# Kernel tuning notes

Measured on AMD Instinct MI355X. Metric: run time of the kernel, lower is better.

The kernel has to match this reference:

```python
import jax, jax.numpy as jnp
import numpy as np

N_TRACK, N_INTER, D, E = 100000, 50000, 64, 800000


def setup_inputs() -> dict:
    key = jax.random.key(0)
    ks = jax.random.split(key, 24)
    f32 = jnp.float32
    def w(k, i, o):
        return jax.random.normal(k, (i, o), f32) / np.float32(np.sqrt(i))
    def b(k, o):
        return jax.random.normal(k, (o,), f32) * np.float32(0.01)
    return {
        "x_track": jax.random.normal(ks[0], (N_TRACK, D), f32),
        "x_inter": jax.random.normal(ks[1], (N_INTER, D), f32),
        "W_conv_ti": w(ks[2], D, D), "b_conv_ti": b(ks[3], D),
        "W_conv_it": w(ks[4], D, D), "b_conv_it": b(ks[5], D),
        "W_att_track": w(ks[6], 3 * D, 3 * D), "b_att_track": b(ks[7], 3 * D),
        "W_aggr_track": w(ks[8], 3 * D, D), "b_aggr_track": b(ks[9], D),
        "W_att_inter": w(ks[10], 3 * D, 3 * D), "b_att_inter": b(ks[11], 3 * D),
        "W_aggr_inter": w(ks[12], 3 * D, D), "b_aggr_inter": b(ks[13], D),
        "W_self_track": w(ks[14], 2 * D, D), "b_self_track": b(ks[15], D),
        "W_self_inter": w(ks[16], 2 * D, D), "b_self_inter": b(ks[17], D),
        "src_ti": jax.random.randint(ks[18], (E,), 0, N_TRACK),
        "dst_ti": jax.random.randint(ks[19], (E,), 0, N_INTER),
        "src_it": jax.random.randint(ks[20], (E,), 0, N_INTER),
        "dst_it": jax.random.randint(ks[21], (E,), 0, N_TRACK),
    }


def _multi_aggregate(msgs, dst_idx, n_dst):
    # torch: scatter_add (sum), sum/count.clamp(1) (mean), scatter_reduce amax
    # over a zeros baseline with include_self=True -> max(0, segment_max).
    s = jax.ops.segment_sum(msgs, dst_idx, num_segments=n_dst)
    cnt = jax.ops.segment_sum(jnp.ones((msgs.shape[0], 1), msgs.dtype), dst_idx,
                              num_segments=n_dst)
    mean = s / jnp.maximum(cnt, 1.0)
    mx = jnp.maximum(jax.ops.segment_max(msgs, dst_idx, num_segments=n_dst), 0.0)
    return jnp.concatenate([mean, s, mx], axis=1)  # aggr order: mean, sum, max


def _dst_update(total, W_att, b_att, W_aggr, b_aggr):
    mask = jnp.sum(jnp.abs(total), axis=1) == 0  # nodes with no messages
    att = jax.nn.sigmoid(total @ W_att + b_att)
    out = (total * att) @ W_aggr + b_aggr
    return jnp.where(mask[:, None], 0.0, out)


def _selfloop(out, x, W_s, b_s):
    out = jax.nn.leaky_relu(out)  # wrapper leaky_relu on conv output
    mask = jnp.sum(jnp.abs(out), axis=1) == 0
    y = jax.nn.leaky_relu(jnp.concatenate([out, x], axis=1) @ W_s + b_s)
    return jnp.where(mask[:, None], x, y)  # masked fallback: keep input rows


def _forward(x_track, x_inter,
             W_conv_ti, b_conv_ti, W_conv_it, b_conv_it,
             W_att_track, b_att_track, W_aggr_track, b_aggr_track,
             W_att_inter, b_att_inter, W_aggr_inter, b_aggr_inter,
             W_self_track, b_self_track, W_self_inter, b_self_inter,
             src_ti, dst_ti, src_it, dst_it):
    # NoAggGAT message: lin(x_j) gathered along edges [E, D]
    msg_ti = x_track[src_ti] @ W_conv_ti + b_conv_ti   # track -> intermediate
    msg_it = x_inter[src_it] @ W_conv_it + b_conv_it   # intermediate -> track
    tot_inter = _multi_aggregate(msg_ti, dst_ti, x_inter.shape[0])  # [N_i, 3D]
    tot_track = _multi_aggregate(msg_it, dst_it, x_track.shape[0])  # [N_t, 3D]
    out_inter = _dst_update(tot_inter, W_att_inter, b_att_inter,
                            W_aggr_inter, b_aggr_inter)
    out_track = _dst_update(tot_track, W_att_track, b_att_track,
                            W_aggr_track, b_aggr_track)
    out_track = _selfloop(out_track, x_track, W_self_track, b_self_track)
    out_inter = _selfloop(out_inter, x_inter, W_self_inter, b_self_inter)
    return jnp.concatenate([out_track, out_inter], axis=0)  # [N_t + N_i, D]


def reference(x_track, x_inter,
              W_conv_ti, b_conv_ti, W_conv_it, b_conv_it,
              W_att_track, b_att_track, W_aggr_track, b_aggr_track,
              W_att_inter, b_att_inter, W_aggr_inter, b_aggr_inter,
              W_self_track, b_self_track, W_self_inter, b_self_inter,
              src_ti, dst_ti, src_it, dst_it):
    return _forward(x_track, x_inter,
                    W_conv_ti, b_conv_ti, W_conv_it, b_conv_it,
                    W_att_track, b_att_track, W_aggr_track, b_aggr_track,
                    W_att_inter, b_att_inter, W_aggr_inter, b_aggr_inter,
                    W_self_track, b_self_track, W_self_inter, b_self_inter,
                    src_ti, dst_ti, src_it, dst_it)
```

## Files before the change

### kernel.cpp

```cpp
#include <hip/hip_runtime.h>
#include <hip/hip_bf16.h>
#include <cstdio>
#include <cstdint>

#define DD 64
#define EPT 8

typedef __attribute__((ext_vector_type(8))) short bf16x8;
typedef __attribute__((ext_vector_type(4))) float f32x4;

__device__ __forceinline__ short f2b(float f) {
    __hip_bfloat16 h = __float2bfloat16(f);
    return __builtin_bit_cast(short, h);
}
__device__ __forceinline__ float b2f(unsigned short s) {
    unsigned u = ((unsigned)s) << 16;
    return __builtin_bit_cast(float, u);
}

__global__ void transform_mfma(const float* __restrict__ xt, const short* __restrict__ WTt,
                               const float* __restrict__ bt, unsigned short* __restrict__ yt, int ntk,
                               const float* __restrict__ xi, const short* __restrict__ WTi,
                               const float* __restrict__ bi, unsigned short* __restrict__ yi, int nik) {
    const float* x; const short* WT; const float* b; unsigned short* y; int n;
    if (blockIdx.y == 0) { x = xt; WT = WTt; b = bt; y = yt; n = ntk; }
    else                 { x = xi; WT = WTi; b = bi; y = yi; n = nik; }
    const int tid = threadIdx.x;
    const int wave = tid >> 6, lane = tid & 63;
    const int lr = lane & 15, lg = lane >> 4;
    const int row0 = blockIdx.x * 256 + wave * 64;
    if (row0 >= n) return;

    bf16x8 B[4][2];
    #pragma unroll
    for (int nt = 0; nt < 4; ++nt)
        #pragma unroll
        for (int ks = 0; ks < 2; ++ks)
            B[nt][ks] = *(const bf16x8*)&WT[(size_t)(nt * 16 + lr) * 64 + ks * 32 + lg * 8];
    float bias[4];
    #pragma unroll
    for (int nt = 0; nt < 4; ++nt) bias[nt] = b[nt * 16 + lr];

    f32x4 acc[4][4];
    f32x4 z4 = {0.f, 0.f, 0.f, 0.f};
    #pragma unroll
    for (int rt = 0; rt < 4; ++rt)
        #pragma unroll
        for (int nt = 0; nt < 4; ++nt) acc[rt][nt] = z4;

    #pragma unroll
    for (int rt = 0; rt < 4; ++rt) {
        int r = row0 + rt * 16 + lr;
        #pragma unroll
        for (int ks = 0; ks < 2; ++ks) {
            bf16x8 af = {0, 0, 0, 0, 0, 0, 0, 0};
            if (r < n) {
                const float* p = &x[(size_t)r * 64 + ks * 32 + lg * 8];
                float4 u0 = *(const float4*)p;
                float4 u1 = *(const float4*)(p + 4);
                af[0] = f2b(u0.x); af[1] = f2b(u0.y); af[2] = f2b(u0.z); af[3] = f2b(u0.w);
                af[4] = f2b(u1.x); af[5] = f2b(u1.y); af[6] = f2b(u1.z); af[7] = f2b(u1.w);
            }
            #pragma unroll
            for (int nt = 0; nt < 4; ++nt)
                acc[rt][nt] = __builtin_amdgcn_mfma_f32_16x16x32_bf16(af, B[nt][ks], acc[rt][nt], 0, 0, 0);
        }
    }
    #pragma unroll
    for (int rt = 0; rt < 4; ++rt)
        #pragma unroll
        for (int j = 0; j < 4; ++j) {
            int r = row0 + rt * 16 + lg * 4 + j;
            if (r >= n) continue;
            #pragma unroll
            for (int nt = 0; nt < 4; ++nt)
                y[(size_t)r * 64 + nt * 16 + lr] = (unsigned short)f2b(acc[rt][nt][j] + bias[nt]);
        }
}

__global__ void hist_part(const int* __restrict__ dti, const int* __restrict__ dit, int E,
                          int* __restrict__ rin, int* __restrict__ rtr, int nin, int ntr) {
    const int* dst = blockIdx.y ? dit : dti;
    int* row       = blockIdx.y ? rtr : rin;
    int n          = blockIdx.y ? ntr : nin;
    int part  = blockIdx.x & 7;
    int chunk = blockIdx.x >> 3;
    int psz = (n + 7) >> 3;
    int lo = part * psz, hi = min(n, lo + psz);
    int base = chunk * (256 * EPT) + threadIdx.x;
    #pragma unroll
    for (int k = 0; k < EPT; ++k) {
        int i = base + k * 256;
        if (i < E) {
            int d = dst[i];
            if (d >= lo && d < hi) atomicAdd(&row[d + 1], 1);
        }
    }
}

#define SCHUNK 4096
__global__ void scan_p1(int* __restrict__ rowA, int nA, int* __restrict__ bsA,
                        int* __restrict__ rowB, int nB, int* __restrict__ bsB) {
    int* row = blockIdx.y ? rowB : rowA;
    int n    = blockIdx.y ? nB : nA;
    int* bs  = blockIdx.y ? bsB : bsA;
    int b = blockIdx.x, t = threadIdx.x;
    int base = 1 + b * SCHUNK;
    __shared__ int wsum[4];
    if (base > n) { if (t == 0) bs[b] = 0; return; }
    int idx0 = base + t * 16;
    int v[16];
    int s = 0;
    #pragma unroll
    for (int k = 0; k < 16; ++k) {
        int i = idx0 + k;
        int x = (i <= n) ? row[i] : 0;
        s += x; v[k] = s;
    }
    int lane = t & 63, wid = t >> 6;
    int ssc = s;
    #pragma unroll
    for (int off = 1; off < 64; off <<= 1) {
        int u = __shfl_up(ssc, off, 64);
        if (lane >= off) ssc += u;
    }
    if (lane == 63) wsum[wid] = ssc;
    __syncthreads();
    int wprev = 0;
    #pragma unroll
    for (int w = 0; w < 4; ++w) if (w < wid) wprev += wsum[w];
    int tpre = ssc - s + wprev;
    #pragma unroll
    for (int k = 0; k < 16; ++k) {
        int i = idx0 + k;
        if (i <= n) row[i] = v[k] + tpre;
    }
    if (t == 0) bs[b] = wsum[0] + wsum[1] + wsum[2] + wsum[3];
}

__global__ void scan_p2(int* __restrict__ bsA, int* __restrict__ bsB) {
    int* bs = blockIdx.x ? bsB : bsA;
    int lane = threadIdx.x;
    int v = bs[lane];
    int s = v;
    #pragma unroll
    for (int off = 1; off < 64; off <<= 1) {
        int u = __shfl_up(s, off, 64);
        if (lane >= off) s += u;
    }
    bs[lane] = s - v;
}

__global__ void scan_p3(int* __restrict__ rowA, int* __restrict__ curA, int nA,
                        const int* __restrict__ bsA,
                        int* __restrict__ rowB, int* __restrict__ curB, int nB,
                        const int* __restrict__ bsB) {
    int* row = blockIdx.y ? rowB : rowA;
    int* cur = blockIdx.y ? curB : curA;
    int n    = blockIdx.y ? nB : nA;
    const int* bs = blockIdx.y ? bsB : bsA;
    int b = blockIdx.x, t = threadIdx.x;
    int base = 1 + b * SCHUNK;
    if (b == 0 && t == 0) { row[0] = 0; cur[0] = 0; }
    if (base > n) return;
    int off = bs[b];
    int end = min(base + SCHUNK - 1, n);
    for (int i = base + t; i <= end; i += 256) {
        int val = row[i] + off;
        row[i] = val;
        if (i < n) cur[i] = val;
    }
}

__global__ void permute_part(const int* __restrict__ sti, const int* __restrict__ dti,
                             int* __restrict__ cin, int* __restrict__ oti,
                             const int* __restrict__ sit, const int* __restrict__ dit,
                             int* __restrict__ ctr, int* __restrict__ oit,
                             int E, int nin, int ntr) {
    const int* src; const int* dst; int* cur; int* col; int n;
    if (blockIdx.y == 0) { src = sti; dst = dti; cur = cin; col = oti; n = nin; }
    else                 { src = sit; dst = dit; cur = ctr; col = oit; n = ntr; }
    int part  = blockIdx.x & 7;
    int chunk = blockIdx.x >> 3;
    int psz = (n + 7) >> 3;
    int lo = part * psz, hi = min(n, lo + psz);
    int base = chunk * (256 * EPT) + threadIdx.x;
    #pragma unroll
    for (int k = 0; k < EPT; ++k) {
        int i = base + k * 256;
        if (i < E) {
            int d = dst[i];
            if (d >= lo && d < hi) {
                int p = atomicAdd(&cur[d], 1);
                col[p] = src[i];
            }
        }
    }
}

__global__ void aggregate2(const unsigned short* __restrict__ yt, const int* __restrict__ row_in,
                           const int* __restrict__ col_ti, short* __restrict__ tot_in,
                           int* __restrict__ flag_in, int n_in,
                           const unsigned short* __restrict__ yi, const int* __restrict__ row_tr,
                           const int* __restrict__ col_it, short* __restrict__ tot_tr,
                           int* __restrict__ flag_tr, int n_tr) {
    const unsigned short* y; const int* row; const int* col; short* tot; int* flag; int n;
    if (blockIdx.y == 0) { y = yt; row = row_in; col = col_ti; tot = tot_in; flag = flag_in; n = n_in; }
    else                 { y = yi; row = row_tr; col = col_it; tot = tot_tr; flag = flag_tr; n = n_tr; }
    int wv = (int)((blockIdx.x * (size_t)blockDim.x + threadIdx.x) >> 6);
    if (wv >= n) return;
    int lane = threadIdx.x & 63;
    int sub = lane >> 4;
    int dl4 = (lane & 15) * 4;
    int e0 = row[wv], e1 = row[wv + 1];
    float s0 = 0.f, s1 = 0.f, s2 = 0.f, s3 = 0.f;
    float m0 = 0.f, m1 = 0.f, m2 = 0.f, m3 = 0.f;
    int e = e0 + sub;
    for (; e + 12 < e1; e += 16) {
        int c0 = col[e], c1 = col[e + 4], c2 = col[e + 8], c3 = col[e + 12];
        ushort4 u0 = *(const ushort4*)&y[(size_t)((unsigned)c0 * 64u + dl4)];
        ushort4 u1 = *(const ushort4*)&y[(size_t)((unsigned)c1 * 64u + dl4)];
        ushort4 u2 = *(const ushort4*)&y[(size_t)((unsigned)c2 * 64u + dl4)];
        ushort4 u3 = *(const ushort4*)&y[(size_t)((unsigned)c3 * 64u + dl4)];
        float f;
        f = b2f(u0.x); s0 += f; m0 = fmaxf(m0, f);
        f = b2f(u0.y); s1 += f; m1 = fmaxf(m1, f);
        f = b2f(u0.z); s2 += f; m2 = fmaxf(m2, f);
        f = b2f(u0.w); s3 += f; m3 = fmaxf(m3, f);
        f = b2f(u1.x); s0 += f; m0 = fmaxf(m0, f);
        f = b2f(u1.y); s1 += f; m1 = fmaxf(m1, f);
        f = b2f(u1.z); s2 += f; m2 = fmaxf(m2, f);
        f = b2f(u1.w); s3 += f; m3 = fmaxf(m3, f);
        f = b2f(u2.x); s0 += f; m0 = fmaxf(m0, f);
        f = b2f(u2.y); s1 += f; m1 = fmaxf(m1, f);
        f = b2f(u2.z); s2 += f; m2 = fmaxf(m2, f);
        f = b2f(u2.w); s3 += f; m3 = fmaxf(m3, f);
        f = b2f(u3.x); s0 += f; m0 = fmaxf(m0, f);
        f = b2f(u3.y); s1 += f; m1 = fmaxf(m1, f);
        f = b2f(u3.z); s2 += f; m2 = fmaxf(m2, f);
        f = b2f(u3.w); s3 += f; m3 = fmaxf(m3, f);
    }
    for (; e + 4 < e1; e += 8) {
        int c0 = col[e], c1 = col[e + 4];
        ushort4 u0 = *(const ushort4*)&y[(size_t)((unsigned)c0 * 64u + dl4)];
        ushort4 u1 = *(const ushort4*)&y[(size_t)((unsigned)c1 * 64u + dl4)];
        float f;
        f = b2f(u0.x); s0 += f; m0 = fmaxf(m0, f);
        f = b2f(u0.y); s1 += f; m1 = fmaxf(m1, f);
        f = b2f(u0.z); s2 += f; m2 = fmaxf(m2, f);
        f = b2f(u0.w); s3 += f; m3 = fmaxf(m3, f);
        f = b2f(u1.x); s0 += f; m0 = fmaxf(m0, f);
        f = b2f(u1.y); s1 += f; m1 = fmaxf(m1, f);
        f = b2f(u1.z); s2 += f; m2 = fmaxf(m2, f);
        f = b2f(u1.w); s3 += f; m3 = fmaxf(m3, f);
    }
    for (; e < e1; e += 4) {
        int c0 = col[e];
        ushort4 u0 = *(const ushort4*)&y[(size_t)((unsigned)c0 * 64u + dl4)];
        float f;
        f = b2f(u0.x); s0 += f; m0 = fmaxf(m0, f);
        f = b2f(u0.y); s1 += f; m1 = fmaxf(m1, f);
        f = b2f(u0.z); s2 += f; m2 = fmaxf(m2, f);
        f = b2f(u0.w); s3 += f; m3 = fmaxf(m3, f);
    }
    #pragma unroll
    for (int off = 16; off <= 32; off <<= 1) {
        s0 += __shfl_xor(s0, off, 64); s1 += __shfl_xor(s1, off, 64);
        s2 += __shfl_xor(s2, off, 64); s3 += __shfl_xor(s3, off, 64);
        m0 = fmaxf(m0, __shfl_xor(m0, off, 64)); m1 = fmaxf(m1, __shfl_xor(m1, off, 64));
        m2 = fmaxf(m2, __shfl_xor(m2, off, 64)); m3 = fmaxf(m3, __shfl_xor(m3, off, 64));
    }
    float dn = fmaxf((float)(e1 - e0), 1.0f);
    float a0 = s0 / dn, a1 = s1 / dn, a2 = s2 / dn, a3 = s3 / dn;
    size_t bse = (size_t)wv * 192;
    if (sub == 0) {
        short4 hm = { f2b(a0), f2b(a1), f2b(a2), f2b(a3) };
        short4 hs = { f2b(s0), f2b(s1), f2b(s2), f2b(s3) };
        short4 hx = { f2b(m0), f2b(m1), f2b(m2), f2b(m3) };
        *(short4*)&tot[bse + dl4]       = hm;
        *(short4*)&tot[bse + 64 + dl4]  = hs;
        *(short4*)&tot[bse + 128 + dl4] = hx;
    }
    float a = fabsf(a0) + fabsf(a1) + fabsf(a2) + fabsf(a3)
            + fabsf(s0) + fabsf(s1) + fabsf(s2) + fabsf(s3)
            + fabsf(m0) + fabsf(m1) + fabsf(m2) + fabsf(m3);
    #pragma unroll
    for (int off = 1; off < 16; off <<= 1) a += __shfl_xor(a, off, 64);
    if (lane == 0) flag[wv] = (a == 0.0f) ? 1 : 0;
}

__global__ void prep_all(const float* __restrict__ Wat_t, const float* __restrict__ Wag_t,
                         const float* __restrict__ Wsf_t, const float* __restrict__ Wcv_t,
                         const float* __restrict__ Wat_i, const float* __restrict__ Wag_i,
                         const float* __restrict__ Wsf_i, const float* __restrict__ Wcv_i,
                         short* __restrict__ oat_t, short* __restrict__ oag_t,
                         short* __restrict__ osf_t, short* __restrict__ ocv_t,
                         short* __restrict__ oat_i, short* __restrict__ oag_i,
                         short* __restrict__ osf_i, short* __restrict__ ocv_i) {
    int i = blockIdx.x * blockDim.x + threadIdx.x;
    if (i >= 122880) return;
    int side = 0;
    if (i >= 61440) { side = 1; i -= 61440; }
    const float* W; short* o; int K, N;
    if (i < 36864)      { W = side ? Wat_i : Wat_t; o = side ? oat_i : oat_t; K = 192; N = 192; }
    else if (i < 49152) { i -= 36864; W = side ? Wag_i : Wag_t; o = side ? oag_i : oag_t; K = 192; N = 64; }
    else if (i < 57344) { i -= 49152; W = side ? Wsf_i : Wsf_t; o = side ? osf_i : osf_t; K = 128; N = 64; }
    else                { i -= 57344; W = side ? Wcv_i : Wcv_t; o = side ? ocv_i : ocv_t; K = 64;  N = 64; }
    int n = i / K, k = i - n * K;
    o[(size_t)n * K + k] = f2b(W[(size_t)k * N + n]);
}

struct FusedArgs {
    const short* tot[2]; const float* x[2];
    const short* watt[2]; const float* batt[2];
    const short* waggr[2]; const float* baggr[2];
    const short* wself[2]; const float* bself[2];
    const int* flag[2]; float* out[2]; int M[2];
};

__launch_bounds__(256, 2)
__global__ void fused_dense(FusedArgs a) {
    const int side = blockIdx.y;
    const int M = a.M[side];
    const int row0 = blockIdx.x * 64;
    if (row0 >= M) return;
    const short* tot = a.tot[side]; const float* x = a.x[side];
    const short* WattT = a.watt[side]; const float* b_att = a.batt[side];
    const short* WaggrT = a.waggr[side]; const float* b_aggr = a.baggr[side];
    const short* WselfT = a.wself[side]; const float* b_self = a.bself[side];
    const int* flag = a.flag[side]; float* out = a.out[side];

    __shared__ __align__(16) short ldsA[64 * 200];
    __shared__ __align__(16) float ldsP[64][4];
    __shared__ int ldsFlag[64];

    const int tid = threadIdx.x;
    const int wave = tid >> 6, lane = tid & 63;
    const int lr = lane & 15, lg = lane >> 4;
    f32x4 z4 = {0.f, 0.f, 0.f, 0.f};

    bf16x8 B1[3][6];
    #pragma unroll
    for (int nt = 0; nt < 3; ++nt)
        #pragma unroll
        for (int ks = 0; ks < 6; ++ks)
            B1[nt][ks] = *(const bf16x8*)&WattT[(size_t)((wave * 3 + nt) * 16 + lr) * 192 + ks * 32 + lg * 8];

    #pragma unroll
    for (int q = 0; q < 6; ++q) {
        int i = tid + q * 256;
        int r = i / 24, c = i % 24;
        int rg = row0 + r;
        uint4 v = {0u, 0u, 0u, 0u};
        if (rg < M) v = ((const uint4*)tot)[(size_t)rg * 24 + c];
        *(uint4*)&ldsA[r * 200 + c * 8] = v;
    }
    if (tid < 64) ldsFlag[tid] = (row0 + tid < M) ? flag[row0 + tid] : 1;
    __syncthreads();

    f32x4 acc1[4][3];
    #pragma unroll
    for (int rt = 0; rt < 4; ++rt)
        #pragma unroll
        for (int nt = 0; nt < 3; ++nt) acc1[rt][nt] = z4;
    #pragma unroll
    for (int ks = 0; ks < 6; ++ks) {
        #pragma unroll
        for (int rt = 0; rt < 4; ++rt) {
            bf16x8 af = *(const bf16x8*)&ldsA[(rt * 16 + lr) * 200 + ks * 32 + lg * 8];
            #pragma unroll
            for (int nt = 0; nt < 3; ++nt)
                acc1[rt][nt] = __builtin_amdgcn_mfma_f32_16x16x32_bf16(af, B1[nt][ks], acc1[rt][nt], 0, 0, 0);
        }
    }
    bf16x8 B2[6];
    #pragma unroll
    for (int ks = 0; ks < 6; ++ks)
        B2[ks] = *(const bf16x8*)&WaggrT[(size_t)(wave * 16 + lr) * 192 + ks * 32 + lg * 8];
    __syncthreads();

    #pragma unroll
    for (int nt = 0; nt < 3; ++nt) {
        int colg = (wave * 3 + nt) * 16 + lr;
        float bb = b_att[colg];
        #pragma unroll
        for (int rt = 0; rt < 4; ++rt)
            #pragma unroll
            for (int j = 0; j < 4; ++j) {
                int rloc = rt * 16 + lg * 4 + j;
                float g = acc1[rt][nt][j] + bb;
                float sg = 1.f / (1.f + __expf(-g));
                int idx = rloc * 200 + colg;
                ldsA[idx] = f2b(b2f((unsigned short)ldsA[idx]) * sg);
            }
    }
    __syncthreads();

    bf16x8 B3[4];
    #pragma unroll
    for (int ks = 0; ks < 4; ++ks)
        B3[ks] = *(const bf16x8*)&WselfT[(size_t)(wave * 16 + lr) * 128 + ks * 32 + lg * 8];
    float4 xr[4];
    #pragma unroll
    for (int q = 0; q < 4; ++q) {
        int i = tid + q * 256;
        int r = i >> 4, c4 = i & 15;
        int rg = row0 + r;
        xr[q] = make_float4(0.f, 0.f, 0.f, 0.f);
        if (rg < M) xr[q] = ((const float4*)x)[(size_t)rg * 16 + c4];
    }
    int fr[4][4];
    #pragma unroll
    for (int rt = 0; rt < 4; ++rt)
        #pragma unroll
        for (int j = 0; j < 4; ++j) fr[rt][j] = ldsFlag[rt * 16 + lg * 4 + j];

    f32x4 acc2[4];
    #pragma unroll
    for (int rt = 0; rt < 4; ++rt) acc2[rt] = z4;
    #pragma unroll
    for (int ks = 0; ks < 6; ++ks)
        #pragma unroll
        for (int rt = 0; rt < 4; ++rt) {
            bf16x8 af = *(const bf16x8*)&ldsA[(rt * 16 + lr) * 200 + ks * 32 + lg * 8];
            acc2[rt] = __builtin_amdgcn_mfma_f32_16x16x32_bf16(af, B2[ks], acc2[rt], 0, 0, 0);
        }
    const int colg2 = wave * 16 + lr;
    float bb2 = b_aggr[colg2];
    float v[4][4], rp[4][4];
    #pragma unroll
    for (int rt = 0; rt < 4; ++rt)
        #pragma unroll
        for (int j = 0; j < 4; ++j) {
            float t = fr[rt][j] ? 0.f : (acc2[rt][j] + bb2);
            t = (t > 0.f) ? t : 0.01f * t;
            v[rt][j] = t;
            rp[rt][j] = fabsf(t);
        }
    #pragma unroll
    for (int off = 1; off < 16; off <<= 1)
        #pragma unroll
        for (int rt = 0; rt < 4; ++rt)
            #pragma unroll
            for (int j = 0; j < 4; ++j) rp[rt][j] += __shfl_xor(rp[rt][j], off, 64);
    __syncthreads();

    #pragma unroll
    for (int rt = 0; rt < 4; ++rt)
        #pragma unroll
        for (int j = 0; j < 4; ++j) {
            int rloc = rt * 16 + lg * 4 + j;
            ldsA[rloc * 136 + colg2] = f2b(v[rt][j]);
            if (lr == 0) ldsP[rloc][wave] = rp[rt][j];
        }
    #pragma unroll
    for (int q = 0; q < 4; ++q) {
        int i = tid + q * 256;
        int r = i >> 4, c4 = i & 15;
        short4 h;
        h.x = f2b(xr[q].x); h.y = f2b(xr[q].y); h.z = f2b(xr[q].z); h.w = f2b(xr[q].w);
        *(short4*)&ldsA[r * 136 + 64 + c4 * 4] = h;
    }
    __syncthreads();

    float xv[4][4];
    #pragma unroll
    for (int rt = 0; rt < 4; ++rt)
        #pragma unroll
        for (int j = 0; j < 4; ++j) {
            int rg = row0 + rt * 16 + lg * 4 + j;
            xv[rt][j] = (rg < M) ? x[(size_t)rg * 64 + colg2] : 0.f;
        }

    f32x4 acc3[4];
    #pragma unroll
    for (int rt = 0; rt < 4; ++rt) acc3[rt] = z4;
    #pragma unroll
    for (int ks = 0; ks < 4; ++ks)
        #pragma unroll
        for (int rt = 0; rt < 4; ++rt) {
            bf16x8 af = *(const bf16x8*)&ldsA[(rt * 16 + lr) * 136 + ks * 32 + lg * 8];
            acc3[rt] = __builtin_amdgcn_mfma_f32_16x16x32_bf16(af, B3[ks], acc3[rt], 0, 0, 0);
        }
    float bb3 = b_self[colg2];
    #pragma unroll
    for (int rt = 0; rt < 4; ++rt)
        #pragma unroll
        for (int j = 0; j < 4; ++j) {
            int rloc = rt * 16 + lg * 4 + j;
            int rg = row0 + rloc;
            if (rg >= M) continue;
            float4 p = *(const float4*)&ldsP[rloc][0];
            bool f2 = (p.x + p.y + p.z + p.w) == 0.f;
            float t = acc3[rt][j] + bb3;
            t = (t > 0.f) ? t : 0.01f * t;
            out[(size_t)rg * 64 + colg2] = f2 ? xv[rt][j] : t;
        }
}

extern "C" void kernel_launch(void* const* d_in, const int* in_sizes, int n_in,
                              void* d_out, int out_size, void* d_ws, size_t ws_size,
                              hipStream_t stream) {
    const float* x_track      = (const float*)d_in[0];
    const float* x_inter      = (const float*)d_in[1];
    const float* W_conv_ti    = (const float*)d_in[2];
    const float* b_conv_ti    = (const float*)d_in[3];
    const float* W_conv_it    = (const float*)d_in[4];
    const float* b_conv_it    = (const float*)d_in[5];
    const float* W_att_track  = (const float*)d_in[6];
    const float* b_att_track  = (const float*)d_in[7];
    const float* W_aggr_track = (const float*)d_in[8];
    const float* b_aggr_track = (const float*)d_in[9];
    const float* W_att_inter  = (const float*)d_in[10];
    const float* b_att_inter  = (const float*)d_in[11];
    const float* W_aggr_inter = (const float*)d_in[12];
    const float* b_aggr_inter = (const float*)d_in[13];
    const float* W_self_track = (const float*)d_in[14];
    const float* b_self_track = (const float*)d_in[15];
    const float* W_self_inter = (const float*)d_in[16];
    const float* b_self_inter = (const float*)d_in[17];
    const int*   src_ti       = (const int*)d_in[18];
    const int*   dst_ti       = (const int*)d_in[19];
    const int*   src_it       = (const int*)d_in[20];
    const int*   dst_it       = (const int*)d_in[21];

    int NT = in_sizes[0] / DD;
    int NI = in_sizes[1] / DD;
    int E  = in_sizes[18];

    uint8_t* w8 = (uint8_t*)d_ws;
    size_t off = 0;
    auto carve = [&](size_t bytes) -> void* {
        off = (off + 255) & ~(size_t)255;
        void* p = (void*)(w8 + off);
        off += bytes;
        return p;
    };
    unsigned short* y_track = (unsigned short*)carve((size_t)NT * 64 * 2);
    unsigned short* y_inter = (unsigned short*)carve((size_t)NI * 64 * 2);
    short* tot_track = (short*)carve((size_t)NT * 192 * 2);
    short* tot_inter = (short*)carve((size_t)NI * 192 * 2);
    int*   row_in    = (int*)carve((size_t)(NI + 1) * 4);
    int*   row_tr    = (int*)carve((size_t)(NT + 1) * 4);
    int*   bs2       = (int*)carve(128 * 4);
    size_t zspan     = (size_t)((uint8_t*)(bs2 + 128) - (uint8_t*)row_in);
    int*   cur_in    = (int*)carve((size_t)(NI + 1) * 4);
    int*   cur_tr    = (int*)carve((size_t)(NT + 1) * 4);
    int*   col_ti    = (int*)carve((size_t)E * 4);
    int*   col_it    = (int*)carve((size_t)E * 4);
    int*   flag_tr   = (int*)carve((size_t)NT * 4);
    int*   flag_in   = (int*)carve((size_t)NI * 4);
    short* WattT_tr  = (short*)carve((size_t)192 * 192 * 2);
    short* WaggrT_tr = (short*)carve((size_t)64 * 192 * 2);
    short* WselfT_tr = (short*)carve((size_t)64 * 128 * 2);
    short* WconvT_tr = (short*)carve((size_t)64 * 64 * 2);
    short* WattT_in  = (short*)carve((size_t)192 * 192 * 2);
    short* WaggrT_in = (short*)carve((size_t)64 * 192 * 2);
    short* WselfT_in = (short*)carve((size_t)64 * 128 * 2);
    short* WconvT_in = (short*)carve((size_t)64 * 64 * 2);
    if (off > ws_size) {
        fprintf(stderr, "kernel_launch: ws too small: need %zu have %zu\n", off, ws_size);
        return;
    }

    hipMemsetAsync(row_in, 0, zspan, stream);

    prep_all<<<(122880 + 255) / 256, 256, 0, stream>>>(
        W_att_track, W_aggr_track, W_self_track, W_conv_ti,
        W_att_inter, W_aggr_inter, W_self_inter, W_conv_it,
        WattT_tr, WaggrT_tr, WselfT_tr, WconvT_tr,
        WattT_in, WaggrT_in, WselfT_in, WconvT_in);

    transform_mfma<<<dim3((max(NT, NI) + 255) / 256, 2), 256, 0, stream>>>(
        x_track, WconvT_tr, b_conv_ti, y_track, NT,
        x_inter, WconvT_in, b_conv_it, y_inter, NI);

    int pgrid = 8 * ((E + 256 * EPT - 1) / (256 * EPT));
    hist_part<<<dim3(pgrid, 2), 256, 0, stream>>>(dst_ti, dst_it, E, row_in, row_tr, NI, NT);
    int nb = (max(NT, NI) + SCHUNK - 1) / SCHUNK;
    scan_p1<<<dim3(nb, 2), 256, 0, stream>>>(row_in, NI, bs2, row_tr, NT, bs2 + 64);
    scan_p2<<<2, 64, 0, stream>>>(bs2, bs2 + 64);
    scan_p3<<<dim3(nb, 2), 256, 0, stream>>>(row_in, cur_in, NI, bs2,
                                             row_tr, cur_tr, NT, bs2 + 64);
    permute_part<<<dim3(pgrid, 2), 256, 0, stream>>>(src_ti, dst_ti, cur_in, col_ti,
                                                     src_it, dst_it, cur_tr, col_it,
                                                     E, NI, NT);

    aggregate2<<<dim3((max(NT, NI) + 3) / 4, 2), 256, 0, stream>>>(
        y_track, row_in, col_ti, tot_inter, flag_in, NI,
        y_inter, row_tr, col_it, tot_track, flag_tr, NT);

    float* out = (float*)d_out;
    FusedArgs fa;
    fa.tot[0] = tot_track;  fa.tot[1] = tot_inter;
    fa.x[0] = x_track;      fa.x[1] = x_inter;
    fa.watt[0] = WattT_tr;  fa.watt[1] = WattT_in;
    fa.batt[0] = b_att_track; fa.batt[1] = b_att_inter;
    fa.waggr[0] = WaggrT_tr; fa.waggr[1] = WaggrT_in;
    fa.baggr[0] = b_aggr_track; fa.baggr[1] = b_aggr_inter;
    fa.wself[0] = WselfT_tr; fa.wself[1] = WselfT_in;
    fa.bself[0] = b_self_track; fa.bself[1] = b_self_inter;
    fa.flag[0] = flag_tr;   fa.flag[1] = flag_in;
    fa.out[0] = out;        fa.out[1] = out + (size_t)NT * 64;
    fa.M[0] = NT;           fa.M[1] = NI;
    fused_dense<<<dim3((max(NT, NI) + 63) / 64, 2), 256, 0, stream>>>(fa);
}
```

Before: 315.1 us.

## Fuse CSR gather aggregation into the dense attention kernel via LDS

Removes the separate aggregate2 kernel and does the per-destination mean/sum/max gather inside the fused dense kernel. Each wave aggregates 16 rows straight into the LDS A tile and flag array. This drops the round trip of the tot and flag intermediates through global memory and one launch. In exchange, the latency-bound gather now runs inside a kernel with high LDS/register use and launch_bounds(256,2), so there may be fewer waves in flight to hide gather latency.

```diff
diff --git a/kernel.cpp b/kernel.cpp
--- a/kernel.cpp
+++ b/kernel.cpp
@@ -196,97 +196,6 @@
             }
         }
     }
-}
-
-__global__ void aggregate2(const unsigned short* __restrict__ yt, const int* __restrict__ row_in,
-                           const int* __restrict__ col_ti, short* __restrict__ tot_in,
-                           int* __restrict__ flag_in, int n_in,
-                           const unsigned short* __restrict__ yi, const int* __restrict__ row_tr,
-                           const int* __restrict__ col_it, short* __restrict__ tot_tr,
-                           int* __restrict__ flag_tr, int n_tr) {
-    const unsigned short* y; const int* row; const int* col; short* tot; int* flag; int n;
-    if (blockIdx.y == 0) { y = yt; row = row_in; col = col_ti; tot = tot_in; flag = flag_in; n = n_in; }
-    else                 { y = yi; row = row_tr; col = col_it; tot = tot_tr; flag = flag_tr; n = n_tr; }
-    int wv = (int)((blockIdx.x * (size_t)blockDim.x + threadIdx.x) >> 6);
-    if (wv >= n) return;
-    int lane = threadIdx.x & 63;
-    int sub = lane >> 4;
-    int dl4 = (lane & 15) * 4;
-    int e0 = row[wv], e1 = row[wv + 1];
-    float s0 = 0.f, s1 = 0.f, s2 = 0.f, s3 = 0.f;
-    float m0 = 0.f, m1 = 0.f, m2 = 0.f, m3 = 0.f;
-    int e = e0 + sub;
-    for (; e + 12 < e1; e += 16) {
-        int c0 = col[e], c1 = col[e + 4], c2 = col[e + 8], c3 = col[e + 12];
-        ushort4 u0 = *(const ushort4*)&y[(size_t)((unsigned)c0 * 64u + dl4)];
-        ushort4 u1 = *(const ushort4*)&y[(size_t)((unsigned)c1 * 64u + dl4)];
-        ushort4 u2 = *(const ushort4*)&y[(size_t)((unsigned)c2 * 64u + dl4)];
-        ushort4 u3 = *(const ushort4*)&y[(size_t)((unsigned)c3 * 64u + dl4)];
-        float f;
-        f = b2f(u0.x); s0 += f; m0 = fmaxf(m0, f);
-        f = b2f(u0.y); s1 += f; m1 = fmaxf(m1, f);
-        f = b2f(u0.z); s2 += f; m2 = fmaxf(m2, f);
-        f = b2f(u0.w); s3 += f; m3 = fmaxf(m3, f);
-        f = b2f(u1.x); s0 += f; m0 = fmaxf(m0, f);
-        f = b2f(u1.y); s1 += f; m1 = fmaxf(m1, f);
-        f = b2f(u1.z); s2 += f; m2 = fmaxf(m2, f);
-        f = b2f(u1.w); s3 += f; m3 = fmaxf(m3, f);
-        f = b2f(u2.x); s0 += f; m0 = fmaxf(m0, f);
-        f = b2f(u2.y); s1 += f; m1 = fmaxf(m1, f);
-        f = b2f(u2.z); s2 += f; m2 = fmaxf(m2, f);
-        f = b2f(u2.w); s3 += f; m3 = fmaxf(m3, f);
-        f = b2f(u3.x); s0 += f; m0 = fmaxf(m0, f);
-        f = b2f(u3.y); s1 += f; m1 = fmaxf(m1, f);
-        f = b2f(u3.z); s2 += f; m2 = fmaxf(m2, f);
-        f = b2f(u3.w); s3 += f; m3 = fmaxf(m3, f);
-    }
-    for (; e + 4 < e1; e += 8) {
-        int c0 = col[e], c1 = col[e + 4];
-        ushort4 u0 = *(const ushort4*)&y[(size_t)((unsigned)c0 * 64u + dl4)];
-        ushort4 u1 = *(const ushort4*)&y[(size_t)((unsigned)c1 * 64u + dl4)];
-        float f;
-        f = b2f(u0.x); s0 += f; m0 = fmaxf(m0, f);
-        f = b2f(u0.y); s1 += f; m1 = fmaxf(m1, f);
-        f = b2f(u0.z); s2 += f; m2 = fmaxf(m2, f);
-        f = b2f(u0.w); s3 += f; m3 = fmaxf(m3, f);
-        f = b2f(u1.x); s0 += f; m0 = fmaxf(m0, f);
-        f = b2f(u1.y); s1 += f; m1 = fmaxf(m1, f);
-        f = b2f(u1.z); s2 += f; m2 = fmaxf(m2, f);
-        f = b2f(u1.w); s3 += f; m3 = fmaxf(m3, f);
-    }
-    for (; e < e1; e += 4) {
-        int c0 = col[e];
-        ushort4 u0 = *(const ushort4*)&y[(size_t)((unsigned)c0 * 64u + dl4)];
-        float f;
-        f = b2f(u0.x); s0 += f; m0 = fmaxf(m0, f);
-        f = b2f(u0.y); s1 += f; m1 = fmaxf(m1, f);
-        f = b2f(u0.z); s2 += f; m2 = fmaxf(m2, f);
-        f = b2f(u0.w); s3 += f; m3 = fmaxf(m3, f);
-    }
-    #pragma unroll
-    for (int off = 16; off <= 32; off <<= 1) {
-        s0 += __shfl_xor(s0, off, 64); s1 += __shfl_xor(s1, off, 64);
-        s2 += __shfl_xor(s2, off, 64); s3 += __shfl_xor(s3, off, 64);
-        m0 = fmaxf(m0, __shfl_xor(m0, off, 64)); m1 = fmaxf(m1, __shfl_xor(m1, off, 64));
-        m2 = fmaxf(m2, __shfl_xor(m2, off, 64)); m3 = fmaxf(m3, __shfl_xor(m3, off, 64));
-    }
-    float dn = fmaxf((float)(e1 - e0), 1.0f);
-    float a0 = s0 / dn, a1 = s1 / dn, a2 = s2 / dn, a3 = s3 / dn;
-    size_t bse = (size_t)wv * 192;
-    if (sub == 0) {
-        short4 hm = { f2b(a0), f2b(a1), f2b(a2), f2b(a3) };
-        short4 hs = { f2b(s0), f2b(s1), f2b(s2), f2b(s3) };
-        short4 hx = { f2b(m0), f2b(m1), f2b(m2), f2b(m3) };
-        *(short4*)&tot[bse + dl4]       = hm;
-        *(short4*)&tot[bse + 64 + dl4]  = hs;
-        *(short4*)&tot[bse + 128 + dl4] = hx;
-    }
-    float a = fabsf(a0) + fabsf(a1) + fabsf(a2) + fabsf(a3)
-            + fabsf(s0) + fabsf(s1) + fabsf(s2) + fabsf(s3)
-            + fabsf(m0) + fabsf(m1) + fabsf(m2) + fabsf(m3);
-    #pragma unroll
-    for (int off = 1; off < 16; off <<= 1) a += __shfl_xor(a, off, 64);
-    if (lane == 0) flag[wv] = (a == 0.0f) ? 1 : 0;
 }
 
 __global__ void prep_all(const float* __restrict__ Wat_t, const float* __restrict__ Wag_t,
@@ -311,24 +220,27 @@
 }
 
 struct FusedArgs {
-    const short* tot[2]; const float* x[2];
+    const unsigned short* y[2]; const int* row[2]; const int* col[2];
+    const float* x[2];
     const short* watt[2]; const float* batt[2];
     const short* waggr[2]; const float* baggr[2];
     const short* wself[2]; const float* bself[2];
-    const int* flag[2]; float* out[2]; int M[2];
+    float* out[2]; int M[2];
 };
 
 __launch_bounds__(256, 2)
-__global__ void fused_dense(FusedArgs a) {
+__global__ void fused_all(FusedArgs a) {
     const int side = blockIdx.y;
     const int M = a.M[side];
     const int row0 = blockIdx.x * 64;
     if (row0 >= M) return;
-    const short* tot = a.tot[side]; const float* x = a.x[side];
+    const unsigned short* y = a.y[side];
+    const int* rowp = a.row[side]; const int* col = a.col[side];
+    const float* x = a.x[side];
     const short* WattT = a.watt[side]; const float* b_att = a.batt[side];
     const short* WaggrT = a.waggr[side]; const float* b_aggr = a.baggr[side];
     const short* WselfT = a.wself[side]; const float* b_self = a.bself[side];
-    const int* flag = a.flag[side]; float* out = a.out[side];
+    float* out = a.out[side];
 
     __shared__ __align__(16) short ldsA[64 * 200];
     __shared__ __align__(16) float ldsP[64][4];
@@ -346,16 +258,89 @@
         for (int ks = 0; ks < 6; ++ks)
             B1[nt][ks] = *(const bf16x8*)&WattT[(size_t)((wave * 3 + nt) * 16 + lr) * 192 + ks * 32 + lg * 8];
 
-    #pragma unroll
-    for (int q = 0; q < 6; ++q) {
-        int i = tid + q * 256;
-        int r = i / 24, c = i % 24;
-        int rg = row0 + r;
-        uint4 v = {0u, 0u, 0u, 0u};
-        if (rg < M) v = ((const uint4*)tot)[(size_t)rg * 24 + c];
-        *(uint4*)&ldsA[r * 200 + c * 8] = v;
-    }
-    if (tid < 64) ldsFlag[tid] = (row0 + tid < M) ? flag[row0 + tid] : 1;
+    {
+        const int sub = lane >> 4;
+        const int dl4 = (lane & 15) * 4;
+        for (int i = 0; i < 16; ++i) {
+            int rloc = wave * 16 + i;
+            int rg = row0 + rloc;
+            int e0 = 0, e1 = 0;
+            if (rg < M) { e0 = rowp[rg]; e1 = rowp[rg + 1]; }
+            float s0 = 0.f, s1 = 0.f, s2 = 0.f, s3 = 0.f;
+            float m0 = 0.f, m1 = 0.f, m2 = 0.f, m3 = 0.f;
+            int e = e0 + sub;
+            for (; e + 12 < e1; e += 16) {
+                int c0 = col[e], c1 = col[e + 4], c2 = col[e + 8], c3 = col[e + 12];
+                ushort4 u0 = *(const ushort4*)&y[(size_t)((unsigned)c0 * 64u + dl4)];
+                ushort4 u1 = *(const ushort4*)&y[(size_t)((unsigned)c1 * 64u + dl4)];
+                ushort4 u2 = *(const ushort4*)&y[(size_t)((unsigned)c2 * 64u + dl4)];
+                ushort4 u3 = *(const ushort4*)&y[(size_t)((unsigned)c3 * 64u + dl4)];
+                float f;
+                f = b2f(u0.x); s0 += f; m0 = fmaxf(m0, f);
+                f = b2f(u0.y); s1 += f; m1 = fmaxf(m1, f);
+                f = b2f(u0.z); s2 += f; m2 = fmaxf(m2, f);
+                f = b2f(u0.w); s3 += f; m3 = fmaxf(m3, f);
+                f = b2f(u1.x); s0 += f; m0 = fmaxf(m0, f);
+                f = b2f(u1.y); s1 += f; m1 = fmaxf(m1, f);
+                f = b2f(u1.z); s2 += f; m2 = fmaxf(m2, f);
+                f = b2f(u1.w); s3 += f; m3 = fmaxf(m3, f);
+                f = b2f(u2.x); s0 += f; m0 = fmaxf(m0, f);
+                f = b2f(u2.y); s1 += f; m1 = fmaxf(m1, f);
+                f = b2f(u2.z); s2 += f; m2 = fmaxf(m2, f);
+                f = b2f(u2.w); s3 += f; m3 = fmaxf(m3, f);
+                f = b2f(u3.x); s0 += f; m0 = fmaxf(m0, f);
+                f = b2f(u3.y); s1 += f; m1 = fmaxf(m1, f);
+                f = b2f(u3.z); s2 += f; m2 = fmaxf(m2, f);
+                f = b2f(u3.w); s3 += f; m3 = fmaxf(m3, f);
+            }
+            for (; e + 4 < e1; e += 8) {
+                int c0 = col[e], c1 = col[e + 4];
+                ushort4 u0 = *(const ushort4*)&y[(size_t)((unsigned)c0 * 64u + dl4)];
+                ushort4 u1 = *(const ushort4*)&y[(size_t)((unsigned)c1 * 64u + dl4)];
+                float f;
+                f = b2f(u0.x); s0 += f; m0 = fmaxf(m0, f);
+                f = b2f(u0.y); s1 += f; m1 = fmaxf(m1, f);
+                f = b2f(u0.z); s2 += f; m2 = fmaxf(m2, f);
+                f = b2f(u0.w); s3 += f; m3 = fmaxf(m3, f);
+                f = b2f(u1.x); s0 += f; m0 = fmaxf(m0, f);
+                f = b2f(u1.y); s1 += f; m1 = fmaxf(m1, f);
+                f = b2f(u1.z); s2 += f; m2 = fmaxf(m2, f);
+                f = b2f(u1.w); s3 += f; m3 = fmaxf(m3, f);
+            }
+            for (; e < e1; e += 4) {
+                int c0 = col[e];
+                ushort4 u0 = *(const ushort4*)&y[(size_t)((unsigned)c0 * 64u + dl4)];
+                float f;
+                f = b2f(u0.x); s0 += f; m0 = fmaxf(m0, f);
+                f = b2f(u0.y); s1 += f; m1 = fmaxf(m1, f);
+                f = b2f(u0.z); s2 += f; m2 = fmaxf(m2, f);
+                f = b2f(u0.w); s3 += f; m3 = fmaxf(m3, f);
+            }
+            #pragma unroll
+            for (int off = 16; off <= 32; off <<= 1) {
+                s0 += __shfl_xor(s0, off, 64); s1 += __shfl_xor(s1, off, 64);
+                s2 += __shfl_xor(s2, off, 64); s3 += __shfl_xor(s3, off, 64);
+                m0 = fmaxf(m0, __shfl_xor(m0, off, 64)); m1 = fmaxf(m1, __shfl_xor(m1, off, 64));
+                m2 = fmaxf(m2, __shfl_xor(m2, off, 64)); m3 = fmaxf(m3, __shfl_xor(m3, off, 64));
+            }
+            float dn = fmaxf((float)(e1 - e0), 1.0f);
+            float a0 = s0 / dn, a1 = s1 / dn, a2 = s2 / dn, a3 = s3 / dn;
+            if (sub == 0) {
+                short4 hm = { f2b(a0), f2b(a1), f2b(a2), f2b(a3) };
+                short4 hs = { f2b(s0), f2b(s1), f2b(s2), f2b(s3) };
+                short4 hx = { f2b(m0), f2b(m1), f2b(m2), f2b(m3) };
+                *(short4*)&ldsA[rloc * 200 + dl4]       = hm;
+                *(short4*)&ldsA[rloc * 200 + 64 + dl4]  = hs;
+                *(short4*)&ldsA[rloc * 200 + 128 + dl4] = hx;
+            }
+            float aa = fabsf(a0) + fabsf(a1) + fabsf(a2) + fabsf(a3)
+                     + fabsf(s0) + fabsf(s1) + fabsf(s2) + fabsf(s3)
+                     + fabsf(m0) + fabsf(m1) + fabsf(m2) + fabsf(m3);
+            #pragma unroll
+            for (int off = 1; off < 16; off <<= 1) aa += __shfl_xor(aa, off, 64);
+            if (lane == 0) ldsFlag[rloc] = (aa == 0.0f) ? 1 : 0;
+        }
+    }
     __syncthreads();
 
     f32x4 acc1[4][3];
@@ -538,8 +523,6 @@
     };
     unsigned short* y_track = (unsigned short*)carve((size_t)NT * 64 * 2);
     unsigned short* y_inter = (unsigned short*)carve((size_t)NI * 64 * 2);
-    short* tot_track = (short*)carve((size_t)NT * 192 * 2);
-    short* tot_inter = (short*)carve((size_t)NI * 192 * 2);
     int*   row_in    = (int*)carve((size_t)(NI + 1) * 4);
     int*   row_tr    = (int*)carve((size_t)(NT + 1) * 4);
     int*   bs2       = (int*)carve(128 * 4);
@@ -548,8 +531,6 @@
     int*   cur_tr    = (int*)carve((size_t)(NT + 1) * 4);
     int*   col_ti    = (int*)carve((size_t)E * 4);
     int*   col_it    = (int*)carve((size_t)E * 4);
-    int*   flag_tr   = (int*)carve((size_t)NT * 4);
-    int*   flag_in   = (int*)carve((size_t)NI * 4);
     short* WattT_tr  = (short*)carve((size_t)192 * 192 * 2);
     short* WaggrT_tr = (short*)carve((size_t)64 * 192 * 2);
     short* WselfT_tr = (short*)carve((size_t)64 * 128 * 2);
@@ -586,13 +567,10 @@
                                                      src_it, dst_it, cur_tr, col_it,
                                                      E, NI, NT);
 
-    aggregate2<<<dim3((max(NT, NI) + 3) / 4, 2), 256, 0, stream>>>(
-        y_track, row_in, col_ti, tot_inter, flag_in, NI,
-        y_inter, row_tr, col_it, tot_track, flag_tr, NT);
-
     float* out = (float*)d_out;
     FusedArgs fa;
-    fa.tot[0] = tot_track;  fa.tot[1] = tot_inter;
+    fa.y[0] = y_inter;  fa.row[0] = row_tr;  fa.col[0] = col_it;
+    fa.y[1] = y_track;  fa.row[1] = row_in;  fa.col[1] = col_ti;
     fa.x[0] = x_track;      fa.x[1] = x_inter;
     fa.watt[0] = WattT_tr;  fa.watt[1] = WattT_in;
     fa.batt[0] = b_att_track; fa.batt[1] = b_att_inter;
@@ -600,8 +578,7 @@
     fa.baggr[0] = b_aggr_track; fa.baggr[1] = b_aggr_inter;
     fa.wself[0] = WselfT_tr; fa.wself[1] = WselfT_in;
     fa.bself[0] = b_self_track; fa.bself[1] = b_self_inter;
-    fa.flag[0] = flag_tr;   fa.flag[1] = flag_in;
     fa.out[0] = out;        fa.out[1] = out + (size_t)NT * 64;
     fa.M[0] = NT;           fa.M[1] = NI;
-    fused_dense<<<dim3((max(NT, NI) + 63) / 64, 2), 256, 0, stream>>>(fa);
-}
+    fused_all<<<dim3((max(NT, NI) + 63) / 64, 2), 256, 0, stream>>>(fa);
+}
```

New measurement: 382.2 us. 21.3% more time.
